# Optimization experiments

Measured on AMD Instinct MI355X. Metric: run time of the kernel, lower is better.

The kernel has to match this reference:

```python
import jax, jax.numpy as jnp
import numpy as np

H = 128
IN = 2048
PROJ = 64
EPS = 1e-5


def setup_inputs() -> dict:
    key = jax.random.key(0)
    ks = jax.random.split(key, 12)
    B, T = 64, 512
    s_in = 1.0 / np.sqrt(H)  # torch RNN init: U(-1/sqrt(H), 1/sqrt(H))
    u = lambda k, shape, s: jax.random.uniform(k, shape, jnp.float32, -s, s)
    return {
        "x": jax.random.normal(ks[0], (B, T, IN), jnp.float32),
        "W_ih1": u(ks[1], (H, IN), s_in),
        "W_hh1": u(ks[2], (H, H), s_in),
        "b_ih1": u(ks[3], (H,), s_in),
        "b_hh1": u(ks[4], (H,), s_in),
        "W_ih2": u(ks[5], (H, H), s_in),
        "W_hh2": u(ks[6], (H, H), s_in),
        "b_ih2": u(ks[7], (H,), s_in),
        "b_hh2": u(ks[8], (H,), s_in),
        "W_proj": u(ks[9], (PROJ, H), 1.0 / np.sqrt(H)),
        "b_proj": u(ks[10], (PROJ,), 1.0 / np.sqrt(H)),
        "gamma": jnp.ones((PROJ,), jnp.float32),
        "beta": jnp.zeros((PROJ,), jnp.float32),
    }


def _rnn(xproj, W_hh, collect):
    # xproj: [B, T, H] = x @ W_ih^T + b_ih + b_hh (biases folded in)
    B = xproj.shape[0]
    h0 = jnp.zeros((B, H), xproj.dtype)
    xs = jnp.swapaxes(xproj, 0, 1)  # [T, B, H]

    def step(h, xp):
        h = jnp.tanh(xp + h @ W_hh.T)
        return h, (h if collect else None)

    h_last, ys = jax.lax.scan(step, h0, xs)
    return h_last, (jnp.swapaxes(ys, 0, 1) if collect else None)


def reference(x, W_ih1, W_hh1, b_ih1, b_hh1, W_ih2, W_hh2, b_ih2, b_hh2,
              W_proj, b_proj, gamma, beta):
    # layer 1: hoist the big input GEMM out of the recurrence
    xp1 = jnp.einsum("bti,hi->bth", x, W_ih1) + (b_ih1 + b_hh1)
    _, y1 = _rnn(xp1, W_hh1, collect=True)  # [B, T, H]
    # layer 2: only final hidden state is needed
    xp2 = jnp.einsum("bth,gh->btg", y1, W_ih2) + (b_ih2 + b_hh2)
    h2, _ = _rnn(xp2, W_hh2, collect=False)  # [B, H]
    # projection + LayerNorm
    z = h2 @ W_proj.T + b_proj  # [B, 64]
    mu = jnp.mean(z, axis=-1, keepdims=True)
    var = jnp.mean((z - mu) ** 2, axis=-1, keepdims=True)
    return (z - mu) * jax.lax.rsqrt(var + EPS) * gamma + beta
```

## Files before the change

### kernel.cpp

```cpp
#include <hip/hip_runtime.h>
#include <math.h>

#define H 128
#define IN 2048
#define PROJ 64
#define BT 32768
#define T_STEPS 512
#define BATCH 64
#define BM 128
#define BKA 64

using f32x4  = __attribute__((ext_vector_type(4))) float;
using bfrag  = __attribute__((ext_vector_type(8))) short;
using h2_t   = __attribute__((ext_vector_type(2))) _Float16;

__device__ __forceinline__ unsigned cvtpk(float lo, float hi) {
  unsigned r;
  asm("v_cvt_pk_bf16_f32 %0, %1, %2" : "=v"(r) : "v"(lo), "v"(hi));
  return r;
}

__global__ __launch_bounds__(512) void xp1_gemm(
    const float* __restrict__ x, const float* __restrict__ W,
    const float* __restrict__ b1, const float* __restrict__ b2,
    float* __restrict__ xp1) {
  __shared__ __align__(16) char As[2][BM * BKA * 2];
  __shared__ __align__(16) char Bs[2][H * BKA * 2];
  const int t  = threadIdx.x;
  const int m0 = blockIdx.x * BM;
  const int wv = t >> 6, l = t & 63;
  const int wm = wv >> 2;
  const int wn = wv & 3;
  const int lr = l & 15;
  const int lq = l >> 4;

  const float* xg[4];
  const float* wg[4];
  int so[4];
#pragma unroll
  for (int i = 0; i < 4; ++i) {
    int c = t + 512 * i, r = c >> 4, k4 = c & 15;
    xg[i] = x + (size_t)(m0 + r) * IN + k4 * 4;
    wg[i] = W + (size_t)r * IN + k4 * 4;
    so[i] = (r * 128 + k4 * 8) ^ ((r & 7) << 4);
  }
  int ao[2][4], bo[2][2];
#pragma unroll
  for (int kf = 0; kf < 2; ++kf) {
#pragma unroll
    for (int mf = 0; mf < 4; ++mf) {
      int r = wm * 64 + mf * 16 + lr;
      ao[kf][mf] = (r * 128 + kf * 64 + lq * 16) ^ ((r & 7) << 4);
    }
#pragma unroll
    for (int nf = 0; nf < 2; ++nf) {
      int r = wn * 32 + nf * 16 + lr;
      bo[kf][nf] = (r * 128 + kf * 64 + lq * 16) ^ ((r & 7) << 4);
    }
  }

  f32x4 acc[4][2];
#pragma unroll
  for (int mf = 0; mf < 4; ++mf)
#pragma unroll
    for (int nf = 0; nf < 2; ++nf)
#pragma unroll
      for (int j = 0; j < 4; ++j) acc[mf][nf][j] = 0.f;

  float4 xr[4], wr[4];
#pragma unroll
  for (int i = 0; i < 4; ++i) {
    xr[i] = *(const float4*)&xg[i][0];
    wr[i] = *(const float4*)&wg[i][0];
  }
#pragma unroll
  for (int i = 0; i < 4; ++i) {
    uint2 ux; ux.x = cvtpk(xr[i].x, xr[i].y); ux.y = cvtpk(xr[i].z, xr[i].w);
    *(uint2*)(As[0] + so[i]) = ux;
    uint2 uw; uw.x = cvtpk(wr[i].x, wr[i].y); uw.y = cvtpk(wr[i].z, wr[i].w);
    *(uint2*)(Bs[0] + so[i]) = uw;
  }
  __syncthreads();

  for (int tc = 0; tc < 32; ++tc) {
    const int kc = (tc + 1) * BKA;
    if (tc < 31) {
#pragma unroll
      for (int i = 0; i < 4; ++i) {
        xr[i] = *(const float4*)&xg[i][kc];
        wr[i] = *(const float4*)&wg[i][kc];
      }
    }
    const char* Ab = As[tc & 1];
    const char* Bb = Bs[tc & 1];
#pragma unroll
    for (int kf = 0; kf < 2; ++kf) {
      bfrag af[4], bf[2];
#pragma unroll
      for (int mf = 0; mf < 4; ++mf) af[mf] = *(const bfrag*)(Ab + ao[kf][mf]);
#pragma unroll
      for (int nf = 0; nf < 2; ++nf) bf[nf] = *(const bfrag*)(Bb + bo[kf][nf]);
#pragma unroll
      for (int mf = 0; mf < 4; ++mf)
#pragma unroll
        for (int nf = 0; nf < 2; ++nf)
          acc[mf][nf] = __builtin_amdgcn_mfma_f32_16x16x32_bf16(
              af[mf], bf[nf], acc[mf][nf], 0, 0, 0);
    }
    if (tc < 31) {
      char* Aw = As[(tc + 1) & 1];
      char* Bw = Bs[(tc + 1) & 1];
#pragma unroll
      for (int i = 0; i < 4; ++i) {
        uint2 ux; ux.x = cvtpk(xr[i].x, xr[i].y); ux.y = cvtpk(xr[i].z, xr[i].w);
        *(uint2*)(Aw + so[i]) = ux;
        uint2 uw; uw.x = cvtpk(wr[i].x, wr[i].y); uw.y = cvtpk(wr[i].z, wr[i].w);
        *(uint2*)(Bw + so[i]) = uw;
      }
    }
    __syncthreads();
  }

#pragma unroll
  for (int nf = 0; nf < 2; ++nf) {
    int n = wn * 32 + nf * 16 + lr;
    float bias = b1[n] + b2[n];
#pragma unroll
    for (int mf = 0; mf < 4; ++mf) {
      int mr = m0 + wm * 64 + mf * 16 + lq * 4;
#pragma unroll
      for (int j = 0; j < 4; ++j)
        xp1[(size_t)(mr + j) * H + n] = acc[mf][nf][j] + bias;
    }
  }
}

struct Wrow { unsigned p0, p1, p2, p3, p4, p5, p6, p7; };

__device__ __forceinline__ float4 gload16(const float* p) {
  float4 r;
  asm volatile("global_load_dwordx4 %0, %1, off" : "=v"(r) : "v"(p));
  return r;
}

__device__ __forceinline__ unsigned pkh(float x, float y) {
  h2_t p = {(_Float16)x, (_Float16)y};
  return __builtin_bit_cast(unsigned, p);
}

__device__ __forceinline__ Wrow packrow(float4 a, float4 b, float4 c,
                                        float4 d) {
  Wrow w = {pkh(a.x, a.y), pkh(a.z, a.w), pkh(b.x, b.y), pkh(b.z, b.w),
            pkh(c.x, c.y), pkh(c.z, c.w), pkh(d.x, d.y), pkh(d.z, d.w)};
  return w;
}

__device__ __forceinline__ float d2(unsigned w, int h, float acc) {
  return __builtin_amdgcn_fdot2(__builtin_bit_cast(h2_t, w),
                                __builtin_bit_cast(h2_t, (unsigned)h), acc,
                                false);
}

__device__ __forceinline__ float dot16(Wrow w, int4 lo, int4 hi, float acc) {
  acc = d2(w.p0, lo.x, acc);
  acc = d2(w.p1, lo.y, acc);
  acc = d2(w.p2, lo.z, acc);
  acc = d2(w.p3, lo.w, acc);
  acc = d2(w.p4, hi.x, acc);
  acc = d2(w.p5, hi.y, acc);
  acc = d2(w.p6, hi.z, acc);
  acc = d2(w.p7, hi.w, acc);
  return acc;
}

template <int CTRL>
__device__ __forceinline__ float dpp_add(float x) {
  return x + __builtin_bit_cast(
                 float, __builtin_amdgcn_mov_dpp(__builtin_bit_cast(int, x),
                                                 CTRL, 0xf, 0xf, true));
}

__device__ __forceinline__ float red8(float v) {
  v = dpp_add<0xB1>(v);
  v = dpp_add<0x4E>(v);
  v = dpp_add<0x141>(v);
  return v;
}

__device__ __forceinline__ float fast_tanh(float x) {
  float e = __expf(2.0f * x);
  return 1.0f - 2.0f / (e + 1.0f);
}

__global__ __launch_bounds__(512)
__attribute__((amdgpu_waves_per_eu(1, 2)))
void rnn_fused(
    const float* __restrict__ xp1,
    const float* __restrict__ W_hh1, const float* __restrict__ W_ih2,
    const float* __restrict__ W_hh2, const float* __restrict__ b_ih2,
    const float* __restrict__ b_hh2, const float* __restrict__ W_proj,
    const float* __restrict__ b_proj, const float* __restrict__ gamma,
    const float* __restrict__ beta, float* __restrict__ out) {
  __shared__ __align__(16) _Float16 h1s[2][H];
  __shared__ __align__(16) _Float16 h2s[2][H];
  const int t = threadIdx.x;
  const int b = blockIdx.x;
  const int l = t & 63;
  const int w = t >> 6;
  const int g = (l >> 3) & 7;
  const int q = l & 7;
  const int r0 = 16 * w + g;
  const int r1 = r0 + 8;

  const float* pA = &W_hh1[r0 * H + 16 * q];
  const float* pB = &W_hh1[r1 * H + 16 * q];
  const float* pC = &W_ih2[r0 * H + 16 * q];
  const float* pD = &W_ih2[r1 * H + 16 * q];
  const float* pE = &W_hh2[r0 * H + 16 * q];
  const float* pF = &W_hh2[r1 * H + 16 * q];
  float4 A0 = gload16(pA), A1 = gload16(pA + 4), A2 = gload16(pA + 8), A3 = gload16(pA + 12);
  float4 B0 = gload16(pB), B1 = gload16(pB + 4), B2 = gload16(pB + 8), B3 = gload16(pB + 12);
  float4 C0 = gload16(pC), C1 = gload16(pC + 4), C2 = gload16(pC + 8), C3 = gload16(pC + 12);
  float4 D0 = gload16(pD), D1 = gload16(pD + 4), D2 = gload16(pD + 8), D3 = gload16(pD + 12);
  float4 E0 = gload16(pE), E1 = gload16(pE + 4), E2 = gload16(pE + 8), E3 = gload16(pE + 12);
  float4 F0 = gload16(pF), F1 = gload16(pF + 4), F2 = gload16(pF + 8), F3 = gload16(pF + 12);
  asm volatile("s_waitcnt vmcnt(0)" ::: "memory");

  Wrow W1r0 = packrow(A0, A1, A2, A3);
  Wrow W1r1 = packrow(B0, B1, B2, B3);
  Wrow W2r0 = packrow(C0, C1, C2, C3);
  Wrow W2r1 = packrow(D0, D1, D2, D3);
  Wrow W3r0 = packrow(E0, E1, E2, E3);
  Wrow W3r1 = packrow(F0, F1, F2, F3);

  const float bias2_0 = b_ih2[r0] + b_hh2[r0];
  const float bias2_1 = b_ih2[r1] + b_hh2[r1];

  if (t < H) { h1s[0][t] = (_Float16)0.f; h2s[0][t] = (_Float16)0.f; }
  __syncthreads();

  const float* xpr0 = xp1 + (size_t)b * T_STEPS * H + r0;
  const float* xpr1 = xpr0 + 8;
  float xpA0 = xpr0[0];
  float xpA1 = xpr1[0];

  for (int ts = 0; ts < T_STEPS; ++ts) {
    const int cur = ts & 1;
    const _Float16* h1p = h1s[cur];
    const _Float16* h2p = h2s[cur];
    _Float16* h1w = h1s[cur ^ 1];
    _Float16* h2w = h2s[cur ^ 1];

    float nx0 = 0.f, nx1 = 0.f;
    if (ts + 1 < T_STEPS) {
      nx0 = xpr0[(size_t)(ts + 1) * H];
      nx1 = xpr1[(size_t)(ts + 1) * H];
    }

    int4 l1 = *(const int4*)&h1p[16 * q];
    int4 u1 = *(const int4*)&h1p[16 * q + 8];
    int4 l2 = *(const int4*)&h2p[16 * q];
    int4 u2 = *(const int4*)&h2p[16 * q + 8];
    float a0 = dot16(W1r0, l1, u1, 0.f);
    float a1 = dot16(W1r1, l1, u1, 0.f);
    float c0 = dot16(W3r0, l2, u2, 0.f);
    float c1 = dot16(W3r1, l2, u2, 0.f);
    a0 = red8(a0); a1 = red8(a1);
    float h1n0 = fast_tanh(xpA0 + a0);
    float h1n1 = fast_tanh(xpA1 + a1);
    if (q == 0) { h1w[r0] = (_Float16)h1n0; h1w[r1] = (_Float16)h1n1; }
    __syncthreads();

    int4 nl = *(const int4*)&h1w[16 * q];
    int4 nu = *(const int4*)&h1w[16 * q + 8];
    float bb0 = dot16(W2r0, nl, nu, c0);
    float bb1 = dot16(W2r1, nl, nu, c1);
    bb0 = red8(bb0); bb1 = red8(bb1);
    float h2n0 = fast_tanh(bias2_0 + bb0);
    float h2n1 = fast_tanh(bias2_1 + bb1);
    if (q == 0) { h2w[r0] = (_Float16)h2n0; h2w[r1] = (_Float16)h2n1; }
    __syncthreads();
    xpA0 = nx0; xpA1 = nx1;
  }

  if (t < PROJ) {
    const float* wp = W_proj + t * H;
    float z = b_proj[t];
#pragma unroll
    for (int i = 0; i < 32; ++i) {
      float4 wv = *(const float4*)&wp[4 * i];
      z = fmaf(wv.x, (float)h2s[0][4 * i + 0], z);
      z = fmaf(wv.y, (float)h2s[0][4 * i + 1], z);
      z = fmaf(wv.z, (float)h2s[0][4 * i + 2], z);
      z = fmaf(wv.w, (float)h2s[0][4 * i + 3], z);
    }
    float s = z;
#pragma unroll
    for (int d = 1; d < 64; d <<= 1) s += __shfl_xor(s, d);
    float mu = s * 0.015625f;
    float dz = z - mu;
    float v = dz * dz;
#pragma unroll
    for (int d = 1; d < 64; d <<= 1) v += __shfl_xor(v, d);
    float rstd = rsqrtf(v * 0.015625f + 1e-5f);
    out[b * PROJ + t] = dz * rstd * gamma[t] + beta[t];
  }
}

extern "C" void kernel_launch(void* const* d_in, const int* in_sizes, int n_in,
                              void* d_out, int out_size, void* d_ws, size_t ws_size,
                              hipStream_t stream) {
  const float* x      = (const float*)d_in[0];
  const float* W_ih1  = (const float*)d_in[1];
  const float* W_hh1  = (const float*)d_in[2];
  const float* b_ih1  = (const float*)d_in[3];
  const float* b_hh1  = (const float*)d_in[4];
  const float* W_ih2  = (const float*)d_in[5];
  const float* W_hh2  = (const float*)d_in[6];
  const float* b_ih2  = (const float*)d_in[7];
  const float* b_hh2  = (const float*)d_in[8];
  const float* W_proj = (const float*)d_in[9];
  const float* b_proj = (const float*)d_in[10];
  const float* gamma  = (const float*)d_in[11];
  const float* beta   = (const float*)d_in[12];

  float* xp1 = (float*)d_ws;

  xp1_gemm<<<BT / BM, 512, 0, stream>>>(x, W_ih1, b_ih1, b_hh1, xp1);
  rnn_fused<<<BATCH, 512, 0, stream>>>(xp1, W_hh1, W_ih2, W_hh2, b_ih2, b_hh2,
                                       W_proj, b_proj, gamma, beta,
                                       (float*)d_out);
}
```

Before: 430.8 us.

## Skew layer-2 recurrence one step behind layer 1 to halve barriers per step

Software-pipelines the two stacked RNN layers so that each iteration computes layer-1 step i and layer-2 step i-1 from the same previously published h1. Both reductions and tanh evaluations now share one barrier per timestep instead of two, and the independent dot products are interleaved for more instruction-level parallelism. A prologue computes the first layer-1 state and an epilogue finishes the last layer-2 step, with the double-buffer indices rearranged to match. The cost is more complex buffer indexing and a small amount of extra prologue and epilogue code.

```diff
diff --git a/kernel.cpp b/kernel.cpp
--- a/kernel.cpp
+++ b/kernel.cpp
@@ -236,51 +236,78 @@
   const float bias2_0 = b_ih2[r0] + b_hh2[r0];
   const float bias2_1 = b_ih2[r1] + b_hh2[r1];
 
-  if (t < H) { h1s[0][t] = (_Float16)0.f; h2s[0][t] = (_Float16)0.f; }
+  if (t < H) { h1s[1][t] = (_Float16)0.f; h2s[1][t] = (_Float16)0.f; }
   __syncthreads();
 
   const float* xpr0 = xp1 + (size_t)b * T_STEPS * H + r0;
   const float* xpr1 = xpr0 + 8;
-  float xpA0 = xpr0[0];
-  float xpA1 = xpr1[0];
-
-  for (int ts = 0; ts < T_STEPS; ++ts) {
-    const int cur = ts & 1;
-    const _Float16* h1p = h1s[cur];
-    const _Float16* h2p = h2s[cur];
-    _Float16* h1w = h1s[cur ^ 1];
-    _Float16* h2w = h2s[cur ^ 1];
+
+  if (q == 0) {
+    h1s[0][r0] = (_Float16)fast_tanh(xpr0[0]);
+    h1s[0][r1] = (_Float16)fast_tanh(xpr1[0]);
+  }
+  __syncthreads();
+
+  float xpc0 = xpr0[H];
+  float xpc1 = xpr1[H];
+
+  for (int i = 1; i < T_STEPS; ++i) {
+    const _Float16* h1p = h1s[(i - 1) & 1];
+    const _Float16* h2p = h2s[i & 1];
+    _Float16* h1w = h1s[i & 1];
+    _Float16* h2w = h2s[(i - 1) & 1];
 
     float nx0 = 0.f, nx1 = 0.f;
-    if (ts + 1 < T_STEPS) {
-      nx0 = xpr0[(size_t)(ts + 1) * H];
-      nx1 = xpr1[(size_t)(ts + 1) * H];
+    if (i + 1 < T_STEPS) {
+      nx0 = xpr0[(size_t)(i + 1) * H];
+      nx1 = xpr1[(size_t)(i + 1) * H];
     }
 
     int4 l1 = *(const int4*)&h1p[16 * q];
     int4 u1 = *(const int4*)&h1p[16 * q + 8];
     int4 l2 = *(const int4*)&h2p[16 * q];
     int4 u2 = *(const int4*)&h2p[16 * q + 8];
+
     float a0 = dot16(W1r0, l1, u1, 0.f);
     float a1 = dot16(W1r1, l1, u1, 0.f);
     float c0 = dot16(W3r0, l2, u2, 0.f);
     float c1 = dot16(W3r1, l2, u2, 0.f);
+    float bb0 = dot16(W2r0, l1, u1, c0);
+    float bb1 = dot16(W2r1, l1, u1, c1);
+
     a0 = red8(a0); a1 = red8(a1);
-    float h1n0 = fast_tanh(xpA0 + a0);
-    float h1n1 = fast_tanh(xpA1 + a1);
-    if (q == 0) { h1w[r0] = (_Float16)h1n0; h1w[r1] = (_Float16)h1n1; }
-    __syncthreads();
-
-    int4 nl = *(const int4*)&h1w[16 * q];
-    int4 nu = *(const int4*)&h1w[16 * q + 8];
-    float bb0 = dot16(W2r0, nl, nu, c0);
-    float bb1 = dot16(W2r1, nl, nu, c1);
     bb0 = red8(bb0); bb1 = red8(bb1);
+
+    float h1n0 = fast_tanh(xpc0 + a0);
+    float h1n1 = fast_tanh(xpc1 + a1);
     float h2n0 = fast_tanh(bias2_0 + bb0);
     float h2n1 = fast_tanh(bias2_1 + bb1);
-    if (q == 0) { h2w[r0] = (_Float16)h2n0; h2w[r1] = (_Float16)h2n1; }
+    if (q == 0) {
+      h1w[r0] = (_Float16)h1n0; h1w[r1] = (_Float16)h1n1;
+      h2w[r0] = (_Float16)h2n0; h2w[r1] = (_Float16)h2n1;
+    }
     __syncthreads();
-    xpA0 = nx0; xpA1 = nx1;
+    xpc0 = nx0; xpc1 = nx1;
+  }
+
+  {
+    const _Float16* h1p = h1s[(T_STEPS - 1) & 1];
+    const _Float16* h2p = h2s[T_STEPS & 1];
+    _Float16* h2w = h2s[(T_STEPS - 1) & 1];
+    int4 l1 = *(const int4*)&h1p[16 * q];
+    int4 u1 = *(const int4*)&h1p[16 * q + 8];
+    int4 l2 = *(const int4*)&h2p[16 * q];
+    int4 u2 = *(const int4*)&h2p[16 * q + 8];
+    float c0 = dot16(W3r0, l2, u2, 0.f);
+    float c1 = dot16(W3r1, l2, u2, 0.f);
+    float bb0 = dot16(W2r0, l1, u1, c0);
+    float bb1 = dot16(W2r1, l1, u1, c1);
+    bb0 = red8(bb0); bb1 = red8(bb1);
+    if (q == 0) {
+      h2w[r0] = (_Float16)fast_tanh(bias2_0 + bb0);
+      h2w[r1] = (_Float16)fast_tanh(bias2_1 + bb1);
+    }
+    __syncthreads();
   }
 
   if (t < PROJ) {
@@ -289,10 +316,10 @@
 #pragma unroll
     for (int i = 0; i < 32; ++i) {
       float4 wv = *(const float4*)&wp[4 * i];
-      z = fmaf(wv.x, (float)h2s[0][4 * i + 0], z);
-      z = fmaf(wv.y, (float)h2s[0][4 * i + 1], z);
-      z = fmaf(wv.z, (float)h2s[0][4 * i + 2], z);
-      z = fmaf(wv.w, (float)h2s[0][4 * i + 3], z);
+      z = fmaf(wv.x, (float)h2s[1][4 * i + 0], z);
+      z = fmaf(wv.y, (float)h2s[1][4 * i + 1], z);
+      z = fmaf(wv.z, (float)h2s[1][4 * i + 2], z);
+      z = fmaf(wv.w, (float)h2s[1][4 * i + 3], z);
     }
     float s = z;
 #pragma unroll
```

Result: faster. 409.9 us (-4.8%).
